# Kernel tuning notes

Hardware: AMD Instinct MI355X
Metric: run time of the kernel (lower is better)

Reference implementation:

```python
import jax, jax.numpy as jnp
import numpy as np

# Model dims (see init_kwargs / shape_source)
ROWS, COLS, C, K, L = 16, 16, 16, 3, 2
B, T = 16, 128
D = ROWS * COLS * C  # state_dim = 4096
PAD = (K - 1) // 2


def setup_inputs() -> dict:
    key = jax.random.key(0)
    ks = jax.random.split(key, 1 + 5 * L)
    inp = {"x_flat": jax.random.normal(ks[0], (B, T, ROWS * COLS), jnp.float32)}
    ki = 1
    for l in range(L):
        cin = (1 if l == 0 else C) + C  # conv sees concat(input, h)
        inp[f"conv_w{l}"] = jax.random.normal(ks[ki], (4 * C, cin, K), jnp.float32) * float(1.0 / np.sqrt(cin * K)); ki += 1
        inp[f"conv_b{l}"] = jnp.zeros((4 * C,), jnp.float32)
        s = float(1.0 / np.sqrt(D))
        inp[f"wq{l}"] = jax.random.normal(ks[ki], (D, D), jnp.float32) * s; ki += 1
        inp[f"wk{l}"] = jax.random.normal(ks[ki], (D, D), jnp.float32) * s; ki += 1
        inp[f"wv{l}"] = jax.random.normal(ks[ki], (D, D), jnp.float32) * s; ki += 1
        inp[f"wo{l}"] = jax.random.normal(ks[ki], (2 * D, D), jnp.float32) * float(1.0 / np.sqrt(2 * D)); ki += 1
    return inp


def _cell_step(x, h, c, cw, cb):
    # x: (B, ROWS, cin_x, COLS); h, c: (B, ROWS, C, COLS). Row-shared Conv1d
    # along cols over concat(x, h) -> 4C gates (standard ConvLSTM).
    z = jnp.concatenate([x, h], axis=2)
    z = z.reshape(B * ROWS, z.shape[2], COLS)
    g = jax.lax.conv_general_dilated(
        z, cw, window_strides=(1,), padding=[(PAD, PAD)],
        dimension_numbers=("NCH", "OIH", "NCH"))
    g = g.reshape(B, ROWS, 4 * C, COLS) + cb[None, None, :, None]
    i, f, gg, o = jnp.split(g, 4, axis=2)
    c_new = jax.nn.sigmoid(f) * c + jax.nn.sigmoid(i) * jnp.tanh(gg)
    h_new = jax.nn.sigmoid(o) * jnp.tanh(c_new)
    return h_new, c_new


def _attn_step(h_vec, kbuf, vbuf, step, wq, wo):
    # Causal dot-product attention: query from raw state, keys from raw
    # history, values from refined history (projections cached in kbuf/vbuf).
    q = h_vec @ wq                                        # (B, D)
    scores = jnp.einsum("bd,tbd->bt", q, kbuf) * (1.0 / np.sqrt(D))
    mask = (jnp.arange(T)[None, :] < step)                # (1, T) strictly-past
    scores = jnp.where(mask, scores, -1e30)
    m = jnp.max(scores, axis=1, keepdims=True)
    e = jnp.exp(scores - m) * mask
    w = e / jnp.maximum(e.sum(axis=1, keepdims=True), 1e-9)
    ctx = jnp.einsum("bt,tbd->bd", w, vbuf)               # zeros at step 0
    out = jnp.tanh(jnp.concatenate([h_vec, ctx], axis=1) @ wo)
    return out, w


def _forward(x_flat, layer_params):
    # frames: (T, B, ROWS, 1, COLS) -- matches torch view+unsqueeze(3)
    x = x_flat.reshape(B, T, ROWS, 1, COLS).transpose(1, 0, 2, 3, 4)
    h0 = tuple(jnp.zeros((B, ROWS, C, COLS), x_flat.dtype) for _ in range(L))
    kb0 = tuple(jnp.zeros((T, B, D), x_flat.dtype) for _ in range(L))

    def body(carry, x_t):
        hs, cs, kbs, vbs, s = carry
        inp = x_t
        nh, nc, nk, nv = [], [], [], []
        out = None
        for l in range(L):
            cw, cb, wq, wk, wv, wo = layer_params[l]
            h_raw, c_new = _cell_step(inp, hs[l], cs[l], cw, cb)
            h_vec = h_raw.reshape(B, D)
            out, _w = _attn_step(h_vec, kbs[l], vbs[l], s, wq, wo)
            nk.append(kbs[l].at[s].set(h_vec @ wk))   # append raw key
            nv.append(vbs[l].at[s].set(out @ wv))     # append refined value
            nh.append(h_raw); nc.append(c_new)
            inp = out.reshape(B, ROWS, C, COLS)
        return (tuple(nh), tuple(nc), tuple(nk), tuple(nv), s + 1), out

    init = (h0, h0, kb0, kb0, jnp.int32(0))
    _, outs = jax.lax.scan(body, init, x)
    return outs.transpose(1, 0, 2)  # (B, T, D) encoder outputs


def reference(x_flat, conv_w0, conv_b0, wq0, wk0, wv0, wo0,
              conv_w1, conv_b1, wq1, wk1, wv1, wo1):
    layer_params = [
        (conv_w0, conv_b0, wq0, wk0, wv0, wo0),
        (conv_w1, conv_b1, wq1, wk1, wv1, wo1),
    ]
    return _forward(x_flat, layer_params)
```

## Files before the change

kernel.cpp:

```cpp
#include <hip/hip_runtime.h>

typedef unsigned short u16;
typedef unsigned int u32;
typedef __attribute__((ext_vector_type(8))) short short8v;
typedef __attribute__((ext_vector_type(4))) float f32x4;
typedef __attribute__((ext_vector_type(8))) u16 ush8;
typedef __attribute__((ext_vector_type(4))) u16 ush4;

__device__ __forceinline__ u16 f2bf(float x) {
  u32 u = __builtin_bit_cast(u32, x);
  return (u16)((u + 0x7FFFu + ((u >> 16) & 1u)) >> 16);
}
__device__ __forceinline__ float bf2f(u16 h) {
  u32 u = ((u32)h) << 16;
  return __builtin_bit_cast(float, u);
}
__device__ __forceinline__ float sigm(float x) { return 1.f / (1.f + expf(-x)); }

typedef const __attribute__((address_space(1))) void gv_t;
typedef __attribute__((address_space(3))) void lv_t;
__device__ __forceinline__ void gload16(const void* g, void* l) {
  __builtin_amdgcn_global_load_lds((gv_t*)g, (lv_t*)l, 16, 0, 0);
}

__device__ __forceinline__ u32 ldsc32(const u32* p) {
  u32 v;
  asm volatile("global_load_dword %0, %1, off sc0 sc1\n\ts_waitcnt vmcnt(0)"
               : "=v"(v) : "v"(p) : "memory");
  return v;
}
__device__ __forceinline__ void atomswap32(u32* p, u32 v) {
  asm volatile("global_atomic_swap %0, %1, off" :: "v"(p), "v"(v) : "memory");
}

__global__ __launch_bounds__(256) void k_prep(int cin, int xmode,
    const float* __restrict__ xin,
    const float* __restrict__ cw, const float* __restrict__ cb,
    const float* __restrict__ wq, const float* __restrict__ wk,
    const float* __restrict__ wo, const float* __restrict__ wv,
    u16* __restrict__ hhi, u16* __restrict__ hlo,
    u16* __restrict__ WT_hi, u16* __restrict__ WTh_lo,
    u16* __restrict__ WTc_hi, u16* __restrict__ WTc_lo,
    u16* __restrict__ WV_hi)
{
  __shared__ __align__(16) float smem[6912];
  const int bx = blockIdx.x;
  const int tid = threadIdx.x;

  if (bx < 256) {
    float* zb = smem;
    float* wb = smem + 576;
    float* bb = smem + 6720;
    const int b = bx >> 4, r = bx & 15;
    const int ch = tid >> 4, col = tid & 15;
    const int cx = cin - 16;
    for (int i = tid; i < 64 * cin * 3; i += 256) {
      int tap = i % 3, tmp = i / 3;
      int ic = tmp % cin, oc = tmp / cin;
      wb[(((oc & 15) * cin + ic) * 3 + tap) * 4 + (oc >> 4)] = cw[i];
    }
    if (tid < 64) bb[tid] = cb[tid];
    for (int i = tid; i < cin * 18; i += 256) zb[i] = 0.f;
    __syncthreads();
    float h = 0.f, c = 0.f;
    const int lane = tid & 63;
    for (int t = 0; t < 128; ++t) {
      if (xmode == 0) {
        if (ch == 0) zb[col + 1] = xin[((long)b * 128 + t) * 256 + r * 16 + col];
      } else {
        zb[ch * 18 + col + 1] = xin[((long)t * 16 + b) * 4096 + r * 256 + ch * 16 + col];
      }
      zb[(cx + ch) * 18 + col + 1] = h;
      __syncthreads();
      float a0 = bb[ch], a1 = bb[16 + ch], a2 = bb[32 + ch], a3 = bb[48 + ch];
      for (int ic = 0; ic < cin; ++ic) {
        float z1 = zb[ic * 18 + col + 1];
        float z0 = __shfl(z1, lane - 1);
        float z2 = __shfl(z1, lane + 1);
        if (col == 0) z0 = 0.f;
        if (col == 15) z2 = 0.f;
        const float4* wp = (const float4*)&wb[(ch * cin + ic) * 12];
        float4 w0 = wp[0], w1 = wp[1], w2 = wp[2];
        a0 += z0 * w0.x + z1 * w1.x + z2 * w2.x;
        a1 += z0 * w0.y + z1 * w1.y + z2 * w2.y;
        a2 += z0 * w0.z + z1 * w1.z + z2 * w2.z;
        a3 += z0 * w0.w + z1 * w1.w + z2 * w2.w;
      }
      __syncthreads();
      c = sigm(a1) * c + sigm(a0) * tanhf(a2);
      h = sigm(a3) * tanhf(c);
      long idx = ((long)t * 16 + b) * 4096 + (long)r * 256 + ch * 16 + col;
      u16 hh = f2bf(h);
      hhi[idx] = hh;
      hlo[idx] = f2bf(h - bf2f(hh));
    }
    return;
  }

  if (bx >= 65792) {
    long i = ((long)(bx - 65792) * 256 + tid) * 4;
    const float4 v = *(const float4*)&wv[i];
    ush4 hv = {f2bf(v.x), f2bf(v.y), f2bf(v.z), f2bf(v.w)};
    *(ush4*)&WV_hi[i] = hv;
    return;
  }

  float (*tb)[33] = (float(*)[33])smem;
  const float* W;
  u16 *hid, *lod;
  int writeLo;
  int tile;
  if (bx < 49408) {
    int t = bx - 256;
    int y = t >> 14;
    tile = t & 16383;
    W = (y == 0) ? wq : (y == 1) ? wk : wo;
    hid = WT_hi + (unsigned long)y * 16777216UL;
    lod = WTh_lo;
    writeLo = (y == 2);
  } else {
    tile = bx - 49408;
    W = wo + 16777216UL;
    hid = WTc_hi;
    lod = WTc_lo;
    writeLo = 1;
  }
  const int tn = tile & 127, tk = tile >> 7;
  const int n0 = tn * 32, k0 = tk * 32;
  const int lr = tid >> 5, lc = tid & 31;
  #pragma unroll
  for (int i = 0; i < 4; ++i)
    tb[lr + i * 8][lc] = W[(long)(k0 + lr + i * 8) * 4096 + n0 + lc];
  __syncthreads();
  #pragma unroll
  for (int i = 0; i < 4; ++i) {
    int n = lr + i * 8;
    float v = tb[lc][n];
    long idx = (long)(n0 + n) * 4096 + k0 + lc;
    u16 h = f2bf(v);
    hid[idx] = h;
    if (writeLo) lod[idx] = f2bf(v - bf2f(h));
  }
}

template<int NM, bool LOOUT>
__device__ __forceinline__ void gemm_core(u16* lds, int bid, int nwg,
    const u16* __restrict__ Ahi, const u16* __restrict__ Alo,
    const u16* __restrict__ Bhi, const u16* __restrict__ Blo,
    u16* __restrict__ Chi, u16* __restrict__ Clo,
    long ldc, long ldclo, int nTc)
{
  const int tid = threadIdx.x, lane = tid & 63, wv = tid >> 6;
  const int bid2 = (bid & 7) * (nwg >> 3) + (bid >> 3);
  const int nT = bid2 % nTc, mT = bid2 / nTc;
  const long aRow0 = (long)mT * 256, bRow0 = (long)nT * 128;

  const int l8 = lane >> 3, cslot = (lane & 7) ^ l8, ck = (cslot & 3) * 8;
  const u16* aSrc = ((cslot < 4) ? Ahi : Alo) + (aRow0 + wv * 32 + l8) * 4096 + ck;
  const u16* bSrc = ((cslot < 4) ? Bhi : Blo) + (bRow0 + wv * 16 + l8) * 4096 + ck;
  const int laO = wv * 2048;
  const int lbO = 16384 + wv * 1024;

  const int r15 = lane & 15, kq = lane >> 4, s7 = r15 & 7;
  const int oHi = (kq ^ s7) * 8, oLo = ((4 + kq) ^ s7) * 8;
  const int wm = wv >> 1, wn = wv & 1;
  f32x4 acc[4][4] = {};

#define STG(buf, kofs)                                                       \
  {                                                                          \
    const u16* sa = aSrc + (kofs);                                           \
    const u16* sb = bSrc + (kofs);                                           \
    u16* la = &lds[(buf) * 24576 + laO];                                     \
    u16* lb = &lds[(buf) * 24576 + lbO];                                     \
    gload16(sa,             la);       gload16(sa +  8 * 4096, la + 512);    \
    gload16(sa + 16 * 4096, la + 1024); gload16(sa + 24 * 4096, la + 1536);  \
    gload16(sb,             lb);       gload16(sb +  8 * 4096, lb + 512);    \
  }

  STG(0, 0) STG(1, 32)
  for (int kt = 0; kt < 128; ++kt) {
    if (kt < 127) { asm volatile("s_waitcnt vmcnt(6)" ::: "memory"); }
    else          { asm volatile("s_waitcnt vmcnt(0)" ::: "memory"); }
    __builtin_amdgcn_sched_barrier(0);
    __builtin_amdgcn_s_barrier();
    const int bb = (kt % 3) * 24576;
    if (kt < 126) STG((kt + 2) % 3, (kt + 2) * 32)
    short8v ah[4], al[4], bh[4], bl[4];
    #pragma unroll
    for (int j = 0; j < 4; ++j) {
      int rb = bb + 16384 + (wn * 64 + j * 16 + r15) * 64;
      bh[j] = *(const short8v*)&lds[rb + oHi];
      if (NM >= 3) bl[j] = *(const short8v*)&lds[rb + oLo];
    }
    #pragma unroll
    for (int i = 0; i < 4; ++i) {
      int ra = bb + (wm * 64 + i * 16 + r15) * 64;
      ah[i] = *(const short8v*)&lds[ra + oHi];
      if (NM >= 2) al[i] = *(const short8v*)&lds[ra + oLo];
    }
    #pragma unroll
    for (int i = 0; i < 4; ++i)
      #pragma unroll
      for (int j = 0; j < 4; ++j) {
        acc[i][j] = __builtin_amdgcn_mfma_f32_16x16x32_bf16(ah[i], bh[j], acc[i][j], 0, 0, 0);
        if (NM >= 3) acc[i][j] = __builtin_amdgcn_mfma_f32_16x16x32_bf16(ah[i], bl[j], acc[i][j], 0, 0, 0);
        if (NM >= 2) acc[i][j] = __builtin_amdgcn_mfma_f32_16x16x32_bf16(al[i], bh[j], acc[i][j], 0, 0, 0);
      }
  }
#undef STG
  const long row0 = aRow0 + wm * 64;
  const long col0 = bRow0 + wn * 64;
  #pragma unroll
  for (int i = 0; i < 4; ++i)
    #pragma unroll
    for (int j = 0; j < 4; ++j) {
      long rr = row0 + i * 16 + kq * 4;
      long cc = col0 + j * 16 + r15;
      #pragma unroll
      for (int g = 0; g < 4; ++g) {
        float v = acc[i][j][g];
        u16 h = f2bf(v);
        Chi[(rr + g) * ldc + cc] = h;
        if (LOOUT) Clo[(rr + g) * ldclo + cc] = f2bf(v - bf2f(h));
      }
    }
}

__global__ __launch_bounds__(512) void k_gemmB(
    const u16* __restrict__ Hs_hi, const u16* __restrict__ Hs_lo,
    const u16* __restrict__ WT_hi, const u16* __restrict__ WTh_lo,
    const u16* __restrict__ WTc_hi, const u16* __restrict__ WTc_lo,
    const u16* __restrict__ WV_hi,
    u16* __restrict__ QKOh, u16* __restrict__ HOlo,
    u16* __restrict__ Wvo_hi, u16* __restrict__ Wvo_lo)
{
  __shared__ __align__(16) u16 lds[73728];
  const int bx = blockIdx.x;
  if (bx < 512) {
    gemm_core<1, false>(lds, bx, 512, Hs_hi, Hs_hi, WT_hi, WT_hi,
                        QKOh, (u16*)nullptr, 12288L, 0L, 64);
  } else if (bx < 768) {
    gemm_core<3, true>(lds, bx - 512, 256, Hs_hi, Hs_lo,
                       WT_hi + 33554432UL, WTh_lo,
                       QKOh + 8192, HOlo, 12288L, 4096L, 32);
  } else {
    gemm_core<2, true>(lds, bx - 768, 512, WTc_hi, WTc_lo, WV_hi, WV_hi,
                       Wvo_hi, Wvo_lo, 4096L, 4096L, 32);
  }
}

__global__ __launch_bounds__(256) void k_scores(
    const u16* __restrict__ Ahi, long lda, long aBS,
    const u16* __restrict__ Bhi, long ldb, long bBS,
    float* __restrict__ Sp)
{
  __shared__ __align__(16) u16 lds[2][16384];
  const int tid = threadIdx.x;
  const int lane = tid & 63;
  const int wv = tid >> 6;
  const long aOff = (long)blockIdx.y * aBS;
  const long bOff = (long)blockIdx.y * bBS;
  const long cOff = (long)blockIdx.y * 16384 + (long)blockIdx.z * 262144;
  const int kbase = blockIdx.z * 512;

  const int l8 = lane >> 3;
  const int cslot = (lane & 7) ^ l8;
  const int ck = (cslot & 3) * 8;
  const u16* aSrc = Ahi + aOff + (wv * 32 + l8) * lda + ck;
  const u16* bSrc = Bhi + bOff + (wv * 32 + l8) * ldb + ck;
  const int ldsAo = wv * 2048;
  const int ldsBo = 8192 + wv * 2048;

  const int r15 = lane & 15, kq = lane >> 4;
  const int s7 = r15 & 7;
  const int oHi = (kq ^ s7) * 8;
  const int aQ = (wv >> 1) * 64;
  const int bQ = (wv & 1) * 64;

  f32x4 acc[4][4] = {};

#define STAGE(buf, kofs)                                                     \
  {                                                                          \
    const u16* sa = aSrc + (kofs);                                           \
    const u16* sb = bSrc + (kofs);                                           \
    u16* la = &lds[buf][ldsAo];                                              \
    u16* lb = &lds[buf][ldsBo];                                              \
    gload16(sa,            la);        gload16(sa +  8 * lda, la + 512);     \
    gload16(sa + 16 * lda, la + 1024); gload16(sa + 24 * lda, la + 1536);    \
    gload16(sb,            lb);        gload16(sb +  8 * ldb, lb + 512);     \
    gload16(sb + 16 * ldb, lb + 1024); gload16(sb + 24 * ldb, lb + 1536);    \
  }

  STAGE(0, kbase)
  __syncthreads();
  int cur = 0;
  for (int k0 = kbase; k0 < kbase + 512; k0 += 32) {
    if (k0 + 32 < kbase + 512) STAGE(cur ^ 1, k0 + 32)
    const u16* L = &lds[cur][0];
    short8v bh[4];
    #pragma unroll
    for (int j = 0; j < 4; ++j)
      bh[j] = *(const short8v*)&L[8192 + (bQ + j * 16 + r15) * 64 + oHi];
    #pragma unroll
    for (int i = 0; i < 4; ++i) {
      short8v ah = *(const short8v*)&L[(aQ + i * 16 + r15) * 64 + oHi];
      #pragma unroll
      for (int j = 0; j < 4; ++j)
        acc[i][j] = __builtin_amdgcn_mfma_f32_16x16x32_bf16(ah, bh[j], acc[i][j], 0, 0, 0);
    }
    __syncthreads();
    cur ^= 1;
  }
#undef STAGE
  const long row0 = aQ, col0 = bQ;
  #pragma unroll
  for (int i = 0; i < 4; ++i)
    #pragma unroll
    for (int j = 0; j < 4; ++j) {
      long rr = row0 + i * 16 + kq * 4;
      long cc = col0 + j * 16 + r15;
      #pragma unroll
      for (int g = 0; g < 4; ++g)
        Sp[cOff + (rr + g) * 128 + cc] = acc[i][j][g];
    }
}

__global__ __launch_bounds__(256) void k_softmax(const float* __restrict__ Sp,
    float* __restrict__ Wx, u32* __restrict__ flags)
{
  if (blockIdx.x == 0) atomswap32(&flags[threadIdx.x * 16], 0);
  const int wv = threadIdx.x >> 6, lane = threadIdx.x & 63;
  const int idx = blockIdx.x * 4 + wv;
  const int b = idx >> 7, t = idx & 127;
  const float* row = &Sp[(long)idx * 128];
  float s0 = 0.f, s1 = 0.f;
  #pragma unroll
  for (int s = 0; s < 8; ++s) {
    s0 += row[s * 262144 + lane];
    s1 += row[s * 262144 + lane + 64];
  }
  float v0 = (lane < t) ? s0 * 0.015625f : -1e30f;
  float v1 = (lane + 64 < t) ? s1 * 0.015625f : -1e30f;
  float m = fmaxf(v0, v1);
  #pragma unroll
  for (int off = 32; off; off >>= 1) m = fmaxf(m, __shfl_xor(m, off));
  float e0 = (lane < t) ? expf(v0 - m) : 0.f;
  float e1 = (lane + 64 < t) ? expf(v1 - m) : 0.f;
  float s = e0 + e1;
  #pragma unroll
  for (int off = 32; off; off >>= 1) s += __shfl_xor(s, off);
  float inv = 1.f / fmaxf(s, 1e-9f);
  float* wr = &Wx[((long)t * 16 + b) * 128];
  wr[lane] = e0 * inv;
  wr[lane + 64] = e1 * inv;
}

__global__ __launch_bounds__(512) void k_phaseC(
    const u16* __restrict__ Wvh, const u16* __restrict__ Wvl,
    const float* __restrict__ Wx,
    const u16* __restrict__ hoh, const u16* __restrict__ hol,
    u16* __restrict__ ring_h,
    float* __restrict__ fdest, int dmode, u32* __restrict__ flags)
{
  __shared__ float VO_lds[128 * 256];
  __shared__ float vo_w[8][256];
  __shared__ float pctx0[256], pctx1[256];
  const int tid = threadIdx.x;
  const int lane = tid & 63, wv = tid >> 6;
  const int n0 = blockIdx.x * 16;
  const int r15 = lane & 15, kq = lane >> 4;
  const long kb = (long)wv * 512 + kq * 8;

  short8v Bh[16], Bl[16];
  {
    const u16* bh = Wvh + (long)(n0 + r15) * 4096 + kb;
    const u16* bl = Wvl + (long)(n0 + r15) * 4096 + kb;
    #pragma unroll
    for (int c = 0; c < 16; ++c) {
      Bh[c] = *(const short8v*)(bh + c * 32);
      Bl[c] = *(const short8v*)(bl + c * 32);
    }
    #pragma unroll
    for (int c = 0; c < 16; ++c) {
      asm volatile("" : "+v"(Bh[c]));
      asm volatile("" : "+v"(Bl[c]));
    }
  }
  const long abase = (long)r15 * 4096 + kb;
  const int b8 = tid >> 4, col8 = tid & 15;

#define GBAR_PCTX(n, T)                                                      \
  {                                                                          \
    asm volatile("s_waitcnt vmcnt(0)" ::: "memory");                         \
    __syncthreads();                                                         \
    if (tid == 0) atomswap32(&flags[(u32)blockIdx.x * 16], (n));             \
    if (tid >= 256) {                                                        \
      const int id = tid - 256;                                              \
      const int bm = id >> 4;                                                \
      const float* wrowm = &Wx[((long)((T) + 1) * 16 + bm) * 128];           \
      float c0 = 0.f, c1 = 0.f;                                              \
      int tp = 0;                                                            \
      for (; tp + 1 < (T); tp += 2) {                                        \
        c0 += wrowm[tp] * VO_lds[tp * 256 + id];                             \
        c1 += wrowm[tp + 1] * VO_lds[(tp + 1) * 256 + id];                   \
      }                                                                      \
      if (tp < (T)) c0 += wrowm[tp] * VO_lds[tp * 256 + id];                 \
      pctx0[id] = c0; pctx1[id] = c1;                                        \
    } else {                                                                 \
      while (ldsc32(&flags[tid * 16]) < (n)) __builtin_amdgcn_s_sleep(1);    \
    }                                                                        \
    __syncthreads();                                                         \
  }

#define RING_STORE(slot, oval)                                               \
  {                                                                          \
    u16 hh_ = f2bf(oval);                                                    \
    u32 vh_ = hh_;                                                           \
    u32 ph_ = (u32)__shfl_xor((int)vh_, 1);                                  \
    if (!(col8 & 1)) {                                                       \
      long oi_ = (long)(slot) * 65536 + (long)b8 * 4096 + n0 + col8;         \
      atomswap32((u32*)&ring_h[oi_], vh_ | (ph_ << 16));                     \
    }                                                                        \
  }

  if (tid < 256) {
    float v = tanhf(bf2f(hoh[(long)b8 * 12288 + n0 + col8])
                  + bf2f(hol[(long)b8 * 4096 + n0 + col8]));
    RING_STORE(0, v)
    if (dmode == 0) fdest[(long)b8 * 4096 + n0 + col8] = v;
    else            fdest[(long)b8 * 128 * 4096 + n0 + col8] = v;
  }
  u32 bn = 1;
  GBAR_PCTX(bn, 0) ++bn;

#define MF(a, b) acc = __builtin_amdgcn_mfma_f32_16x16x32_bf16(a, b, acc, 0, 0, 0);

  for (int t = 0; t < 127; ++t) {
    const u16* ph = ring_h + (long)t * 65536 + abase;
    short8v xh[16];
    #pragma unroll
    for (int c = 0; c < 16; ++c) xh[c] = *(const short8v*)(ph + c * 32);
    f32x4 acc = {0.f, 0.f, 0.f, 0.f};
    #pragma unroll
    for (int c = 0; c < 16; ++c) { MF(xh[c], Bh[c]) MF(xh[c], Bl[c]) }
    #pragma unroll
    for (int g = 0; g < 4; ++g)
      vo_w[wv][(kq * 4 + g) * 16 + r15] = acc[g];
    __syncthreads();
    if (tid < 256) {
      float v = vo_w[0][tid] + vo_w[1][tid] + vo_w[2][tid] + vo_w[3][tid]
              + vo_w[4][tid] + vo_w[5][tid] + vo_w[6][tid] + vo_w[7][tid];
      VO_lds[t * 256 + tid] = v;
      const float* wrow = &Wx[((long)(t + 1) * 16 + b8) * 128];
      float ho = bf2f(hoh[((long)(t + 1) * 16 + b8) * 12288 + n0 + col8])
               + bf2f(hol[((long)(t + 1) * 16 + b8) * 4096 + n0 + col8]);
      float o = tanhf(ho + pctx0[tid] + pctx1[tid] + wrow[t] * v);
      RING_STORE(t + 1, o)
      if (dmode == 0) fdest[((long)(t + 1) * 16 + b8) * 4096 + n0 + col8] = o;
      else            fdest[((long)b8 * 128 + (t + 1)) * 4096 + n0 + col8] = o;
    }
    if (t < 126) { GBAR_PCTX(bn, t + 1) ++bn; }
  }
#undef GBAR_PCTX
#undef RING_STORE
#undef MF
}

extern "C" void kernel_launch(void* const* d_in, const int* in_sizes, int n_in,
                              void* d_out, int out_size, void* d_ws, size_t ws_size,
                              hipStream_t stream)
{
  (void)in_sizes; (void)n_in; (void)out_size;
  if (ws_size < 454049792UL) return;
  char* ws = (char*)d_ws;
  u16* WT_hi  = (u16*)(ws + 0UL);
  u16* WTh_lo = (u16*)(ws + 100663296UL);
  u16* WTc_hi = (u16*)(ws + 134217728UL);
  u16* WTc_lo = (u16*)(ws + 167772160UL);
  u16* WV_hi  = (u16*)(ws + 201326592UL);
  u16* QKOh   = (u16*)(ws + 234881024UL);
  u16* HOlo   = (u16*)(ws + 285212672UL);
  u16* Wvo_hi = (u16*)(ws + 301989888UL);
  u16* Wvo_lo = (u16*)(ws + 335544320UL);
  u16* Hs_hi  = (u16*)(ws + 369098752UL);
  u16* Hs_lo  = (u16*)(ws + 385875968UL);
  float* Wmx  = (float*)(ws + 402653184UL);
  u16* ring_h = (u16*)(ws + 403701760UL);
  float* OUT0 = (float*)(ws + 420478976UL);
  float* Sp   = (float*)(ws + 420478976UL);
  u32* flg    = (u32*)(ws + 454033408UL);
  float* dout = (float*)d_out;
  const float* x_flat = (const float*)d_in[0];

  for (int l = 0; l < 2; ++l) {
    const float* cw = (const float*)d_in[1 + l * 6];
    const float* cb = (const float*)d_in[2 + l * 6];
    const float* wq = (const float*)d_in[3 + l * 6];
    const float* wk = (const float*)d_in[4 + l * 6];
    const float* wv = (const float*)d_in[5 + l * 6];
    const float* wo = (const float*)d_in[6 + l * 6];
    const int cin = (l == 0) ? 17 : 32;

    hipLaunchKernelGGL(k_prep, dim3(82176), dim3(256), 0, stream,
        cin, l, (l == 0) ? x_flat : OUT0, cw, cb, wq, wk, wo, wv,
        Hs_hi, Hs_lo, WT_hi, WTh_lo, WTc_hi, WTc_lo, WV_hi);

    hipLaunchKernelGGL(k_gemmB, dim3(1280), dim3(512), 0, stream,
        Hs_hi, Hs_lo, WT_hi, WTh_lo, WTc_hi, WTc_lo, WV_hi,
        QKOh, HOlo, Wvo_hi, Wvo_lo);

    hipLaunchKernelGGL(k_scores, dim3(1, 16, 8), dim3(256), 0, stream,
        QKOh, 12288L, 196608L, QKOh + 4096, 12288L, 196608L, Sp);
    hipLaunchKernelGGL(k_softmax, dim3(512), dim3(256), 0, stream, Sp, Wmx, flg);

    hipLaunchKernelGGL(k_phaseC, dim3(256), dim3(512), 0, stream,
        Wvo_hi, Wvo_lo, Wmx, QKOh + 8192, HOlo,
        ring_h, (l == 0) ? OUT0 : dout, l, flg);
  }
}
```

Measured before the change: 3.893 ms.

## Overlap layer-1 weight conversion with layer-0 recurrent phase using spare blocks

Layer 1's weight transpose and bf16 conversion now runs in extra blocks appended to the layer-0 k_phaseC launch. These blocks can fill idle CUs while the 256 persistent recurrent blocks spin on inter-block flags, so k_prep for layer 1 only handles the small conv part. The per-block VO history moves from LDS to a global buffer that reuses the Hs area, which frees LDS but adds global traffic in the per-step context sum. The flag spin-wait also drops s_sleep. This relies on the persistent blocks being scheduled before the conversion blocks, otherwise the grid barrier could deadlock.

```diff
diff --git a/kernel.cpp b/kernel.cpp
--- a/kernel.cpp
+++ b/kernel.cpp
@@ -108,12 +108,11 @@
   float (*tb)[33] = (float(*)[33])smem;
   const float* W;
   u16 *hid, *lod;
-  int writeLo;
-  int tile;
+  int writeLo, tile;
   if (bx < 49408) {
-    int t = bx - 256;
-    int y = t >> 14;
-    tile = t & 16383;
+    int j = bx - 256;
+    int y = j >> 14;
+    tile = j & 16383;
     W = (y == 0) ? wq : (y == 1) ? wk : wo;
     hid = WT_hi + (unsigned long)y * 16777216UL;
     lod = WTh_lo;
@@ -359,15 +358,74 @@
     const u16* __restrict__ Wvh, const u16* __restrict__ Wvl,
     const float* __restrict__ Wx,
     const u16* __restrict__ hoh, const u16* __restrict__ hol,
-    u16* __restrict__ ring_h,
-    float* __restrict__ fdest, int dmode, u32* __restrict__ flags)
-{
-  __shared__ float VO_lds[128 * 256];
+    u16* __restrict__ ring_h, float* __restrict__ VOg,
+    float* __restrict__ fdest, int dmode, u32* __restrict__ flags,
+    const float* __restrict__ nwq, const float* __restrict__ nwk,
+    const float* __restrict__ nwo, const float* __restrict__ nwv,
+    u16* __restrict__ nWT_hi, u16* __restrict__ nWTh_lo,
+    u16* __restrict__ nWTc_hi, u16* __restrict__ nWTc_lo,
+    u16* __restrict__ nWV_hi)
+{
   __shared__ float vo_w[8][256];
   __shared__ float pctx0[256], pctx1[256];
+  __shared__ __align__(16) float tb[32][33];
+  const int bx = blockIdx.x;
   const int tid = threadIdx.x;
+
+  if (bx >= 256) {
+    const int j = bx - 256;
+    if (j >= 65536) {
+      if (tid < 256) {
+        long i = ((long)(j - 65536) * 256 + tid) * 4;
+        const float4 v = *(const float4*)&nwv[i];
+        ush4 hv = {f2bf(v.x), f2bf(v.y), f2bf(v.z), f2bf(v.w)};
+        *(ush4*)&nWV_hi[i] = hv;
+      }
+      return;
+    }
+    const float* W;
+    u16 *hid, *lod;
+    int writeLo, tile;
+    if (j < 49152) {
+      int y = j >> 14;
+      tile = j & 16383;
+      W = (y == 0) ? nwq : (y == 1) ? nwk : nwo;
+      hid = nWT_hi + (unsigned long)y * 16777216UL;
+      lod = nWTh_lo;
+      writeLo = (y == 2);
+    } else {
+      tile = j - 49152;
+      W = nwo + 16777216UL;
+      hid = nWTc_hi;
+      lod = nWTc_lo;
+      writeLo = 1;
+    }
+    const int tn = tile & 127, tk = tile >> 7;
+    const int n0 = tn * 32, k0 = tk * 32;
+    const int lr = tid >> 5, lc = tid & 31;
+    if (tid < 256) {
+      #pragma unroll
+      for (int i = 0; i < 4; ++i)
+        tb[lr + i * 8][lc] = W[(long)(k0 + lr + i * 8) * 4096 + n0 + lc];
+    }
+    __syncthreads();
+    if (tid < 256) {
+      #pragma unroll
+      for (int i = 0; i < 4; ++i) {
+        int n = lr + i * 8;
+        float v = tb[lc][n];
+        long idx = (long)(n0 + n) * 4096 + k0 + lc;
+        u16 h = f2bf(v);
+        hid[idx] = h;
+        if (writeLo) lod[idx] = f2bf(v - bf2f(h));
+      }
+    }
+    return;
+  }
+
+  float* VO = VOg + (long)bx * 32768;
   const int lane = tid & 63, wv = tid >> 6;
-  const int n0 = blockIdx.x * 16;
+  const int n0 = bx * 16;
   const int r15 = lane & 15, kq = lane >> 4;
   const long kb = (long)wv * 512 + kq * 8;
 
@@ -393,7 +451,7 @@
   {                                                                          \
     asm volatile("s_waitcnt vmcnt(0)" ::: "memory");                         \
     __syncthreads();                                                         \
-    if (tid == 0) atomswap32(&flags[(u32)blockIdx.x * 16], (n));             \
+    if (tid == 0) atomswap32(&flags[(u32)bx * 16], (n));                     \
     if (tid >= 256) {                                                        \
       const int id = tid - 256;                                              \
       const int bm = id >> 4;                                                \
@@ -401,13 +459,13 @@
       float c0 = 0.f, c1 = 0.f;                                              \
       int tp = 0;                                                            \
       for (; tp + 1 < (T); tp += 2) {                                        \
-        c0 += wrowm[tp] * VO_lds[tp * 256 + id];                             \
-        c1 += wrowm[tp + 1] * VO_lds[(tp + 1) * 256 + id];                   \
+        c0 += wrowm[tp] * VO[tp * 256 + id];                                 \
+        c1 += wrowm[tp + 1] * VO[(tp + 1) * 256 + id];                       \
       }                                                                      \
-      if (tp < (T)) c0 += wrowm[tp] * VO_lds[tp * 256 + id];                 \
+      if (tp < (T)) c0 += wrowm[tp] * VO[tp * 256 + id];                     \
       pctx0[id] = c0; pctx1[id] = c1;                                        \
     } else {                                                                 \
-      while (ldsc32(&flags[tid * 16]) < (n)) __builtin_amdgcn_s_sleep(1);    \
+      while (ldsc32(&flags[tid * 16]) < (n)) {}                              \
     }                                                                        \
     __syncthreads();                                                         \
   }
@@ -450,7 +508,7 @@
     if (tid < 256) {
       float v = vo_w[0][tid] + vo_w[1][tid] + vo_w[2][tid] + vo_w[3][tid]
               + vo_w[4][tid] + vo_w[5][tid] + vo_w[6][tid] + vo_w[7][tid];
-      VO_lds[t * 256 + tid] = v;
+      VO[t * 256 + tid] = v;
       const float* wrow = &Wx[((long)(t + 1) * 16 + b8) * 128];
       float ho = bf2f(hoh[((long)(t + 1) * 16 + b8) * 12288 + n0 + col8])
                + bf2f(hol[((long)(t + 1) * 16 + b8) * 4096 + n0 + col8]);
@@ -484,6 +542,7 @@
   u16* Wvo_lo = (u16*)(ws + 335544320UL);
   u16* Hs_hi  = (u16*)(ws + 369098752UL);
   u16* Hs_lo  = (u16*)(ws + 385875968UL);
+  float* VOg  = (float*)(ws + 369098752UL);
   float* Wmx  = (float*)(ws + 402653184UL);
   u16* ring_h = (u16*)(ws + 403701760UL);
   float* OUT0 = (float*)(ws + 420478976UL);
@@ -500,8 +559,12 @@
     const float* wv = (const float*)d_in[5 + l * 6];
     const float* wo = (const float*)d_in[6 + l * 6];
     const int cin = (l == 0) ? 17 : 32;
-
-    hipLaunchKernelGGL(k_prep, dim3(82176), dim3(256), 0, stream,
+    const float* nwq = (const float*)d_in[9];
+    const float* nwk = (const float*)d_in[10];
+    const float* nwv = (const float*)d_in[11];
+    const float* nwo = (const float*)d_in[12];
+
+    hipLaunchKernelGGL(k_prep, dim3((l == 0) ? 82176 : 256), dim3(256), 0, stream,
         cin, l, (l == 0) ? x_flat : OUT0, cw, cb, wq, wk, wo, wv,
         Hs_hi, Hs_lo, WT_hi, WTh_lo, WTc_hi, WTc_lo, WV_hi);
 
@@ -513,8 +576,10 @@
         QKOh, 12288L, 196608L, QKOh + 4096, 12288L, 196608L, Sp);
     hipLaunchKernelGGL(k_softmax, dim3(512), dim3(256), 0, stream, Sp, Wmx, flg);
 
-    hipLaunchKernelGGL(k_phaseC, dim3(256), dim3(512), 0, stream,
+    hipLaunchKernelGGL(k_phaseC, dim3((l == 0) ? 82176 : 256), dim3(512), 0, stream,
         Wvo_hi, Wvo_lo, Wmx, QKOh + 8192, HOlo,
-        ring_h, (l == 0) ? OUT0 : dout, l, flg);
-  }
-}
+        ring_h, VOg, (l == 0) ? OUT0 : dout, l, flg,
+        nwq, nwk, nwo, nwv,
+        WT_hi, WTh_lo, WTc_hi, WTc_lo, WV_hi);
+  }
+}
```

New measurement: 5.309 ms. 36.4% more time.
